# Performance work log

Hardware: AMD Instinct MI355X
Metric: run time of the kernel (lower is better)

Reference implementation:

```python
import jax, jax.numpy as jnp
import numpy as np
from jax import lax

# physiological constants from the source module
DT = 1.0
TAU_L = 10.0
G_B = 0.6
G_L = 1.0 / TAU_L
LAMBDA_MAX = 0.35
STEPS = int(50 / DT)

IN_SIZE, HID, OUT, BATCH = 1024, 2048, 512, 4096


def setup_inputs() -> dict:
    key = jax.random.key(0)
    k1, k2, k3, k4, k5, k6 = jax.random.split(key, 6)
    psp = jax.random.uniform(k1, (IN_SIZE, BATCH), dtype=jnp.float32)  # |mm(spikes,kernel)| is >=0
    label = jax.random.uniform(k2, (BATCH, OUT), dtype=jnp.float32)    # teaching current I
    # Linear params init: uniform(-0.1, 0.1) as in the torch module
    W_h = jax.random.uniform(k3, (HID, IN_SIZE), minval=-0.1, maxval=0.1, dtype=jnp.float32)
    b_h = jax.random.uniform(k4, (HID,), minval=-0.1, maxval=0.1, dtype=jnp.float32)
    W_o = jax.random.uniform(k5, (OUT, HID), minval=-0.1, maxval=0.1, dtype=jnp.float32)
    b_o = jax.random.uniform(k6, (OUT,), minval=-0.1, maxval=0.1, dtype=jnp.float32)
    return {"psp": psp, "label": label, "W_h": W_h, "b_h": b_h, "W_o": W_o, "b_o": b_o}


def reference(psp, label, W_h, b_h, W_o, b_o):
    a = DT / TAU_L
    gr = G_B / G_L  # = 6.0
    x = psp.T  # [B, in] -- Hidden_layer transposes basal_input
    # psp is constant over the time loop, so the hidden basal GEMM hoists out
    basal_V_h = x @ W_h.T + b_h  # [B, HID]
    soma_h0 = jnp.zeros_like(basal_V_h)
    soma_o0 = jnp.zeros((x.shape[0], W_o.shape[0]), dtype=x.dtype)

    def step(carry, _):
        soma_h, soma_o = carry
        # hidden two-compartment leaky integration
        soma_h = soma_h + a * (-soma_h + gr * (basal_V_h - soma_h))
        rate_h = LAMBDA_MAX * jax.nn.sigmoid(soma_h)  # [B, HID]
        basal_V_o = rate_h @ W_o.T + b_o              # [B, OUT]
        # output layer, training (test=False) branch: nudged by teaching current I=label
        soma_o = soma_o + a * (-soma_o + gr * (basal_V_o - soma_o) + label - soma_o)
        return (soma_h, soma_o), None

    (soma_h, soma_o), _ = lax.scan(step, (soma_h0, soma_o0), None, length=STEPS)
    return LAMBDA_MAX * jax.nn.sigmoid(soma_o)  # out_layer.spike_rate, [B, OUT]
```

## Files before the change

### kernel.cpp

```cpp
#include <hip/hip_runtime.h>
#include <hip/hip_bf16.h>


typedef __bf16 bf16_t;
typedef __bf16 bf16x8 __attribute__((ext_vector_type(8)));
typedef __bf16 bf16x4v __attribute__((ext_vector_type(4)));
typedef float f32x4 __attribute__((ext_vector_type(4)));
typedef float f32x16 __attribute__((ext_vector_type(16)));

#define GLD_TO_LDS16(gp, lp)                                            \
  __builtin_amdgcn_global_load_lds(                                     \
      (__attribute__((address_space(1))) void*)(void*)(gp),             \
      (__attribute__((address_space(3))) void*)(lp), 16, 0, 0)

__global__ __launch_bounds__(256) void prep(
    const float* __restrict__ psp, bf16_t* __restrict__ pspT,
    const float4* __restrict__ w1, bf16x4v* __restrict__ o1, int n1,
    const float4* __restrict__ w2, bf16x4v* __restrict__ o2, int n2) {
  __shared__ float tile[64][65];
  const int tid = threadIdx.x;
  const int b = blockIdx.x;
  const int c0 = (b & 63) * 64;
  const int r0 = (b >> 6) * 64;
  const int tx = tid & 63;
  const int ty = tid >> 6;
#pragma unroll
  for (int i = 0; i < 16; ++i) {
    const int r = ty + i * 4;
    tile[r][tx] = psp[(size_t)(r0 + r) * 4096 + c0 + tx];
  }
  const int base = b * 768 + tid;
#pragma unroll
  for (int i = 0; i < 3; ++i) {
    const int idx = base + i * 256;
    const float4 v = (idx < n1) ? w1[idx] : w2[idx - n1];
    bf16x4v o;
    o.x = (bf16_t)v.x; o.y = (bf16_t)v.y; o.z = (bf16_t)v.z; o.w = (bf16_t)v.w;
    if (idx < n1) o1[idx] = o;
    else if (idx - n1 < n2) o2[idx - n1] = o;
  }
  __syncthreads();
#pragma unroll
  for (int i = 0; i < 16; ++i) {
    const int r = ty + i * 4;
    pspT[(size_t)(c0 + r) * 1024 + r0 + tx] = (bf16_t)tile[tx][r];
  }
}

__global__ __launch_bounds__(256, 4) void gemm1_nt(
    const bf16_t* __restrict__ A, const bf16_t* __restrict__ Bt,
    const float* __restrict__ bias, bf16_t* __restrict__ C,
    int M, int N, int K) {
  constexpr int BK = 64;
  __shared__ __align__(16) bf16_t sA[128 * BK];
  __shared__ __align__(16) bf16_t sB[64 * BK];

  const int tid = threadIdx.x;
  const int wave = tid >> 6;
  const int lane = tid & 63;
  const int bm = blockIdx.x * 128;
  const int bn = blockIdx.y * 64;
  const int wm = (wave & 1) * 64;
  const int wn = (wave >> 1) * 32;

  f32x16 acc[2] = {};

  const int srow8 = lane >> 3;
  const int gseg = (lane & 7) ^ srow8;
  const bf16_t* Ag = A + (size_t)(bm + wave * 32 + srow8) * K + gseg * 8;
  const bf16_t* Bg = Bt + (size_t)(bn + wave * 16 + srow8) * K + gseg * 8;
  const int dstA = wave * 2048;
  const int dstB = wave * 1024;

  const int col = lane & 31;
  const int g = lane >> 5;

  for (int k0 = 0; k0 < K; k0 += BK) {
#pragma unroll
    for (int c = 0; c < 4; ++c)
      GLD_TO_LDS16(Ag + (size_t)(c * 8) * K + k0, sA + dstA + c * 512);
#pragma unroll
    for (int c = 0; c < 2; ++c)
      GLD_TO_LDS16(Bg + (size_t)(c * 8) * K + k0, sB + dstB + c * 512);
    __syncthreads();

#pragma unroll
    for (int ks = 0; ks < 4; ++ks) {
      const int q = ks * 2 + g;
      bf16x8 av[2], bv;
#pragma unroll
      for (int i = 0; i < 2; ++i) {
        const int rr = wm + i * 32 + col;
        av[i] = *(const bf16x8*)(sA + rr * BK + ((q ^ (rr & 7)) * 8));
      }
      {
        const int rr = wn + col;
        bv = *(const bf16x8*)(sB + rr * BK + ((q ^ (rr & 7)) * 8));
      }
#pragma unroll
      for (int i = 0; i < 2; ++i)
        acc[i] = __builtin_amdgcn_mfma_f32_32x32x16_bf16(av[i], bv, acc[i],
                                                         0, 0, 0);
    }
    __syncthreads();
  }

  const int rbase = 4 * g;
  const int gn = bn + wn + col;
  const float bj = bias[gn];
#pragma unroll
  for (int i = 0; i < 2; ++i) {
#pragma unroll
    for (int r = 0; r < 16; ++r) {
      const int gm = bm + wm + i * 32 + (r & 3) + 8 * (r >> 2) + rbase;
      const float z = 0.8571428571428571f * (acc[i][r] + bj);
      C[(size_t)gm * N + gn] = (bf16_t)(0.35f / (1.0f + __expf(-z)));
    }
  }
}

__global__ __launch_bounds__(256, 4) void gemm2_nt(
    const bf16_t* __restrict__ A, const bf16_t* __restrict__ Bt,
    const float* __restrict__ bias, const float* __restrict__ lbl,
    float* __restrict__ out, int M, int N, int K) {
  __shared__ __align__(16) bf16_t sA[2][64 * 64];
  __shared__ __align__(16) bf16_t sB[2][64 * 64];

  const int tid = threadIdx.x;
  const int wave = tid >> 6;
  const int lane = tid & 63;
  const int bm = blockIdx.x * 64;
  const int bn = blockIdx.y * 64;
  const int wm = (wave & 1) * 32;
  const int wn = (wave >> 1) * 32;

  f32x4 acc[2][2] = {};

  const int srow8 = lane >> 3;
  const int gseg = (lane & 7) ^ srow8;
  const bf16_t* Ag = A + (size_t)(bm + wave * 16 + srow8) * K + gseg * 8;
  const bf16_t* Bg = Bt + (size_t)(bn + wave * 16 + srow8) * K + gseg * 8;
  const int dst = wave * 1024;

  const int fr = lane & 15;
  const int qh = lane >> 4;

  for (int k0 = 0; k0 < K; k0 += 128) {
#pragma unroll
    for (int p = 0; p < 2; ++p) {
#pragma unroll
      for (int c = 0; c < 2; ++c) {
        GLD_TO_LDS16(Ag + k0 + p * 64 + (size_t)(c * 8) * K,
                     sA[p] + dst + c * 512);
        GLD_TO_LDS16(Bg + k0 + p * 64 + (size_t)(c * 8) * K,
                     sB[p] + dst + c * 512);
      }
    }
    __syncthreads();

#pragma unroll
    for (int ks = 0; ks < 4; ++ks) {
      const int q = ks * 4 + qh;
      const int pnl = q >> 3;
      const int q2 = q & 7;
      bf16x8 av[2], bv[2];
#pragma unroll
      for (int i = 0; i < 2; ++i) {
        const int ra = wm + i * 16 + fr;
        av[i] = *(const bf16x8*)(sA[pnl] + ra * 64 + ((q2 ^ (ra & 7)) * 8));
      }
#pragma unroll
      for (int j = 0; j < 2; ++j) {
        const int rb = wn + j * 16 + fr;
        bv[j] = *(const bf16x8*)(sB[pnl] + rb * 64 + ((q2 ^ (rb & 7)) * 8));
      }
#pragma unroll
      for (int i = 0; i < 2; ++i)
#pragma unroll
        for (int j = 0; j < 2; ++j)
          acc[i][j] = __builtin_amdgcn_mfma_f32_16x16x32_bf16(
              av[i], bv[j], acc[i][j], 0, 0, 0);
    }
    __syncthreads();
  }

  const int cm0 = qh * 4;
#pragma unroll
  for (int j = 0; j < 2; ++j) {
    const int gn = bn + wn + j * 16 + fr;
    const float bj = bias[gn];
#pragma unroll
    for (int i = 0; i < 2; ++i) {
#pragma unroll
      for (int r = 0; r < 4; ++r) {
        const int gm = bm + wm + i * 16 + cm0 + r;
        const float z =
            0.75f * (acc[i][j][r] + bj) + 0.125f * lbl[(size_t)gm * N + gn];
        out[(size_t)gm * N + gn] = 0.35f / (1.0f + __expf(-z));
      }
    }
  }
}

extern "C" void kernel_launch(void* const* d_in, const int* in_sizes, int n_in,
                              void* d_out, int out_size, void* d_ws, size_t ws_size,
                              hipStream_t stream) {
  constexpr int IN = 1024, HID = 2048, OUT = 512, B = 4096;
  const float* psp = (const float*)d_in[0];
  const float* lbl = (const float*)d_in[1];
  const float* W_h = (const float*)d_in[2];
  const float* b_h = (const float*)d_in[3];
  const float* W_o = (const float*)d_in[4];
  const float* b_o = (const float*)d_in[5];
  float* out = (float*)d_out;

  bf16_t* Whb = (bf16_t*)d_ws;
  bf16_t* Wob = Whb + (size_t)HID * IN;
  bf16_t* pspT = Wob + (size_t)OUT * HID;
  bf16_t* Rm = pspT + (size_t)B * IN;

  prep<<<1024, 256, 0, stream>>>(
      psp, pspT, (const float4*)W_h, (bf16x4v*)Whb, HID * IN / 4,
      (const float4*)W_o, (bf16x4v*)Wob, OUT * HID / 4);
  gemm1_nt<<<dim3(B / 128, HID / 64), 256, 0, stream>>>(
      pspT, Whb, b_h, Rm, B, HID, IN);
  gemm2_nt<<<dim3(B / 64, OUT / 64), 256, 0, stream>>>(
      Rm, Wob, b_o, lbl, out, B, OUT, HID);
}
```

Measured before the change: 129.3 us.

## Enlarge gemm1 tile to 128x256 with triple-buffered LDS pipeline

gemm1 now uses 512-thread blocks, each computing a 128x256 output tile instead of 128x64, with eight waves each owning a 64x64 sub-tile. Global-to-LDS loads for tile t+2 are issued in three chunks interleaved with the four MFMA phases of tile t, using a three-stage LDS ring buffer, explicit vmcnt waits, barriers and setprio around the MFMAs. The intent is to hide global-load latency and raise arithmetic intensity. The cost is more LDS per block, lower occupancy, and hand-tuned waitcnt ordering that could be fragile.

```diff
diff --git a/kernel.cpp b/kernel.cpp
--- a/kernel.cpp
+++ b/kernel.cpp
@@ -47,74 +47,141 @@
   }
 }
 
-__global__ __launch_bounds__(256, 4) void gemm1_nt(
+__global__ __launch_bounds__(512, 2) void gemm1_nt(
     const bf16_t* __restrict__ A, const bf16_t* __restrict__ Bt,
     const float* __restrict__ bias, bf16_t* __restrict__ C,
     int M, int N, int K) {
   constexpr int BK = 64;
-  __shared__ __align__(16) bf16_t sA[128 * BK];
-  __shared__ __align__(16) bf16_t sB[64 * BK];
+  __shared__ __align__(16) bf16_t sA[3][128 * BK];
+  __shared__ __align__(16) bf16_t sB[3][256 * BK];
 
   const int tid = threadIdx.x;
   const int wave = tid >> 6;
   const int lane = tid & 63;
   const int bm = blockIdx.x * 128;
-  const int bn = blockIdx.y * 64;
+  const int bn = blockIdx.y * 256;
   const int wm = (wave & 1) * 64;
-  const int wn = (wave >> 1) * 32;
-
-  f32x16 acc[2] = {};
+  const int wn = (wave >> 1) * 64;
+
+  f32x16 acc[2][2] = {};
 
   const int srow8 = lane >> 3;
   const int gseg = (lane & 7) ^ srow8;
-  const bf16_t* Ag = A + (size_t)(bm + wave * 32 + srow8) * K + gseg * 8;
-  const bf16_t* Bg = Bt + (size_t)(bn + wave * 16 + srow8) * K + gseg * 8;
-  const int dstA = wave * 2048;
-  const int dstB = wave * 1024;
+  const bf16_t* Ag = A + (size_t)(bm + wave * 16 + srow8) * K + gseg * 8;
+  const bf16_t* Bg = Bt + (size_t)(bn + wave * 32 + srow8) * K + gseg * 8;
+  const int dstA = wave * 1024;
+  const int dstB = wave * 2048;
 
   const int col = lane & 31;
   const int g = lane >> 5;
-
-  for (int k0 = 0; k0 < K; k0 += BK) {
-#pragma unroll
-    for (int c = 0; c < 4; ++c)
-      GLD_TO_LDS16(Ag + (size_t)(c * 8) * K + k0, sA + dstA + c * 512);
-#pragma unroll
-    for (int c = 0; c < 2; ++c)
-      GLD_TO_LDS16(Bg + (size_t)(c * 8) * K + k0, sB + dstB + c * 512);
-    __syncthreads();
-
-#pragma unroll
-    for (int ks = 0; ks < 4; ++ks) {
-      const int q = ks * 2 + g;
-      bf16x8 av[2], bv;
-#pragma unroll
-      for (int i = 0; i < 2; ++i) {
-        const int rr = wm + i * 32 + col;
-        av[i] = *(const bf16x8*)(sA + rr * BK + ((q ^ (rr & 7)) * 8));
-      }
-      {
-        const int rr = wn + col;
-        bv = *(const bf16x8*)(sB + rr * BK + ((q ^ (rr & 7)) * 8));
-      }
-#pragma unroll
-      for (int i = 0; i < 2; ++i)
-        acc[i] = __builtin_amdgcn_mfma_f32_32x32x16_bf16(av[i], bv, acc[i],
-                                                         0, 0, 0);
-    }
-    __syncthreads();
-  }
+  const int NT = K / BK;
+
+#define STAGE_A2(bufi, t)                                              \
+  {                                                                    \
+    bf16_t* d_ = &sA[bufi][dstA];                                      \
+    const bf16_t* s_ = Ag + (size_t)(t) * BK;                          \
+    GLD_TO_LDS16(s_, d_);                                              \
+    GLD_TO_LDS16(s_ + (size_t)8 * K, d_ + 512);                        \
+  }
+#define STAGE_B01(bufi, t)                                             \
+  {                                                                    \
+    bf16_t* d_ = &sB[bufi][dstB];                                      \
+    const bf16_t* s_ = Bg + (size_t)(t) * BK;                          \
+    GLD_TO_LDS16(s_, d_);                                              \
+    GLD_TO_LDS16(s_ + (size_t)8 * K, d_ + 512);                        \
+  }
+#define STAGE_B23(bufi, t)                                             \
+  {                                                                    \
+    bf16_t* d_ = &sB[bufi][dstB + 1024];                               \
+    const bf16_t* s_ = Bg + (size_t)(t) * BK + (size_t)16 * K;         \
+    GLD_TO_LDS16(s_, d_);                                              \
+    GLD_TO_LDS16(s_ + (size_t)8 * K, d_ + 512);                        \
+  }
+#define PH_READ(ks)                                                    \
+  {                                                                    \
+    const int q = (ks) * 2 + g;                                        \
+    _Pragma("unroll") for (int i = 0; i < 2; ++i) {                    \
+      const int rr = wm + i * 32 + col;                                \
+      av[i] = *(const bf16x8*)(a_ + rr * BK + ((q ^ (rr & 7)) * 8));   \
+    }                                                                  \
+    _Pragma("unroll") for (int j = 0; j < 2; ++j) {                    \
+      const int rr = wn + j * 32 + col;                                \
+      bv[j] = *(const bf16x8*)(b_ + rr * BK + ((q ^ (rr & 7)) * 8));   \
+    }                                                                  \
+  }
+#define PH_MFMA()                                                      \
+  __builtin_amdgcn_s_setprio(1);                                       \
+  _Pragma("unroll") for (int i = 0; i < 2; ++i)                        \
+      _Pragma("unroll") for (int j = 0; j < 2; ++j)                    \
+          acc[i][j] = __builtin_amdgcn_mfma_f32_32x32x16_bf16(         \
+              av[i], bv[j], acc[i][j], 0, 0, 0);                       \
+  __builtin_amdgcn_s_setprio(0);
+#define SYNC_PRE()                                                     \
+  __builtin_amdgcn_sched_barrier(0);                                   \
+  __builtin_amdgcn_s_barrier();                                        \
+  asm volatile("s_waitcnt lgkmcnt(0)" ::: "memory");                   \
+  __builtin_amdgcn_sched_barrier(0);
+#define SYNC_POST()                                                    \
+  __builtin_amdgcn_sched_barrier(0);                                   \
+  __builtin_amdgcn_s_barrier();                                        \
+  __builtin_amdgcn_sched_barrier(0);
+
+  STAGE_A2(0, 0); STAGE_B01(0, 0); STAGE_B23(0, 0);
+  STAGE_A2(1, 1); STAGE_B01(1, 1); STAGE_B23(1, 1);
+  asm volatile("s_waitcnt vmcnt(6)" ::: "memory");
+  __builtin_amdgcn_sched_barrier(0);
+  __builtin_amdgcn_s_barrier();
+  __builtin_amdgcn_sched_barrier(0);
+
+  int cur = 0;
+  for (int t = 0; t < NT; ++t) {
+    const bf16_t* a_ = sA[cur];
+    const bf16_t* b_ = sB[cur];
+    const int nxt = (cur >= 1) ? cur - 1 : cur + 2;
+    const bool st = (t + 2) < NT;
+    bf16x8 av[2], bv[2];
+
+    PH_READ(0);
+    if (st) STAGE_A2(nxt, t + 2);
+    SYNC_PRE(); PH_MFMA(); SYNC_POST();
+    PH_READ(1);
+    if (st) STAGE_B01(nxt, t + 2);
+    SYNC_PRE(); PH_MFMA(); SYNC_POST();
+    PH_READ(2);
+    if (st) STAGE_B23(nxt, t + 2);
+    SYNC_PRE(); PH_MFMA(); SYNC_POST();
+    PH_READ(3);
+    if (t + 1 < NT) {
+      if (t + 2 < NT)
+        asm volatile("s_waitcnt vmcnt(6)" ::: "memory");
+      else
+        asm volatile("s_waitcnt vmcnt(0)" ::: "memory");
+    }
+    SYNC_PRE(); PH_MFMA(); SYNC_POST();
+
+    cur = (cur + 1 == 3) ? 0 : cur + 1;
+  }
+#undef STAGE_A2
+#undef STAGE_B01
+#undef STAGE_B23
+#undef PH_READ
+#undef PH_MFMA
+#undef SYNC_PRE
+#undef SYNC_POST
 
   const int rbase = 4 * g;
-  const int gn = bn + wn + col;
-  const float bj = bias[gn];
-#pragma unroll
-  for (int i = 0; i < 2; ++i) {
-#pragma unroll
-    for (int r = 0; r < 16; ++r) {
-      const int gm = bm + wm + i * 32 + (r & 3) + 8 * (r >> 2) + rbase;
-      const float z = 0.8571428571428571f * (acc[i][r] + bj);
-      C[(size_t)gm * N + gn] = (bf16_t)(0.35f / (1.0f + __expf(-z)));
+#pragma unroll
+  for (int j = 0; j < 2; ++j) {
+    const int gn = bn + wn + j * 32 + col;
+    const float bj = bias[gn];
+#pragma unroll
+    for (int i = 0; i < 2; ++i) {
+#pragma unroll
+      for (int r = 0; r < 16; ++r) {
+        const int gm = bm + wm + i * 32 + (r & 3) + 8 * (r >> 2) + rbase;
+        const float z = 0.8571428571428571f * (acc[i][j][r] + bj);
+        C[(size_t)gm * N + gn] = (bf16_t)(0.35f / (1.0f + __expf(-z)));
+      }
     }
   }
 }
@@ -222,7 +289,7 @@
   prep<<<1024, 256, 0, stream>>>(
       psp, pspT, (const float4*)W_h, (bf16x4v*)Whb, HID * IN / 4,
       (const float4*)W_o, (bf16x4v*)Wob, OUT * HID / 4);
-  gemm1_nt<<<dim3(B / 128, HID / 64), 256, 0, stream>>>(
+  gemm1_nt<<<dim3(B / 128, HID / 256), 512, 0, stream>>>(
       pspT, Whb, b_h, Rm, B, HID, IN);
   gemm2_nt<<<dim3(B / 64, OUT / 64), 256, 0, stream>>>(
       Rm, Wob, b_o, lbl, out, B, OUT, HID);
```

Result: slower. 132.1 us (+2.1%).

## Double-buffer LDS tiles in both GEMMs to overlap global loads with MFMA

Applied to the files above, without the earlier changes.

Both GEMM kernels now use two LDS buffers. The next K-tile is issued with global_load_lds before the current tile's MFMAs run, and each iteration ends with a single waitcnt plus barrier instead of two syncthreads. MFMA sections are wrapped in s_setprio, and launch-bound occupancy hints are lowered to match the larger LDS footprint. The aim is to hide global load latency behind compute, at the cost of more LDS per block and fewer resident blocks per CU.

```diff
diff --git a/kernel.cpp b/kernel.cpp
--- a/kernel.cpp
+++ b/kernel.cpp
@@ -12,6 +12,12 @@
   __builtin_amdgcn_global_load_lds(                                     \
       (__attribute__((address_space(1))) void*)(void*)(gp),             \
       (__attribute__((address_space(3))) void*)(lp), 16, 0, 0)
+
+#define END_OF_ITER_SYNC()                                              \
+  asm volatile("s_waitcnt vmcnt(0)" ::: "memory");                      \
+  __builtin_amdgcn_sched_barrier(0);                                    \
+  __builtin_amdgcn_s_barrier();                                         \
+  __builtin_amdgcn_sched_barrier(0);
 
 __global__ __launch_bounds__(256) void prep(
     const float* __restrict__ psp, bf16_t* __restrict__ pspT,
@@ -47,13 +53,13 @@
   }
 }
 
-__global__ __launch_bounds__(256, 4) void gemm1_nt(
+__global__ __launch_bounds__(256, 3) void gemm1_nt(
     const bf16_t* __restrict__ A, const bf16_t* __restrict__ Bt,
     const float* __restrict__ bias, bf16_t* __restrict__ C,
     int M, int N, int K) {
   constexpr int BK = 64;
-  __shared__ __align__(16) bf16_t sA[128 * BK];
-  __shared__ __align__(16) bf16_t sB[64 * BK];
+  __shared__ __align__(16) bf16_t sA[2][128 * BK];
+  __shared__ __align__(16) bf16_t sB[2][64 * BK];
 
   const int tid = threadIdx.x;
   const int wave = tid >> 6;
@@ -74,16 +80,29 @@
 
   const int col = lane & 31;
   const int g = lane >> 5;
-
-  for (int k0 = 0; k0 < K; k0 += BK) {
-#pragma unroll
-    for (int c = 0; c < 4; ++c)
-      GLD_TO_LDS16(Ag + (size_t)(c * 8) * K + k0, sA + dstA + c * 512);
-#pragma unroll
-    for (int c = 0; c < 2; ++c)
-      GLD_TO_LDS16(Bg + (size_t)(c * 8) * K + k0, sB + dstB + c * 512);
-    __syncthreads();
-
+  const int NT = K / BK;
+
+#define STAGE1(bufi, t)                                                \
+  {                                                                    \
+    bf16_t* dA_ = &sA[bufi][dstA];                                     \
+    bf16_t* dB_ = &sB[bufi][dstB];                                     \
+    const bf16_t* sa_ = Ag + (size_t)(t) * BK;                         \
+    const bf16_t* sb_ = Bg + (size_t)(t) * BK;                         \
+    _Pragma("unroll") for (int c_ = 0; c_ < 4; ++c_)                   \
+        GLD_TO_LDS16(sa_ + (size_t)(c_ * 8) * K, dA_ + c_ * 512);      \
+    _Pragma("unroll") for (int c_ = 0; c_ < 2; ++c_)                   \
+        GLD_TO_LDS16(sb_ + (size_t)(c_ * 8) * K, dB_ + c_ * 512);      \
+  }
+
+  STAGE1(0, 0);
+  END_OF_ITER_SYNC();
+
+  int cur = 0;
+  for (int t = 0; t < NT; ++t) {
+    if (t + 1 < NT) STAGE1(cur ^ 1, t + 1);
+
+    const bf16_t* a_ = sA[cur];
+    const bf16_t* b_ = sB[cur];
 #pragma unroll
     for (int ks = 0; ks < 4; ++ks) {
       const int q = ks * 2 + g;
@@ -91,19 +110,26 @@
 #pragma unroll
       for (int i = 0; i < 2; ++i) {
         const int rr = wm + i * 32 + col;
-        av[i] = *(const bf16x8*)(sA + rr * BK + ((q ^ (rr & 7)) * 8));
+        av[i] = *(const bf16x8*)(a_ + rr * BK + ((q ^ (rr & 7)) * 8));
       }
       {
         const int rr = wn + col;
-        bv = *(const bf16x8*)(sB + rr * BK + ((q ^ (rr & 7)) * 8));
-      }
+        bv = *(const bf16x8*)(b_ + rr * BK + ((q ^ (rr & 7)) * 8));
+      }
+      __builtin_amdgcn_s_setprio(1);
 #pragma unroll
       for (int i = 0; i < 2; ++i)
         acc[i] = __builtin_amdgcn_mfma_f32_32x32x16_bf16(av[i], bv, acc[i],
                                                          0, 0, 0);
-    }
-    __syncthreads();
-  }
+      __builtin_amdgcn_s_setprio(0);
+    }
+
+    if (t + 1 < NT) {
+      END_OF_ITER_SYNC();
+      cur ^= 1;
+    }
+  }
+#undef STAGE1
 
   const int rbase = 4 * g;
   const int gn = bn + wn + col;
@@ -119,12 +145,12 @@
   }
 }
 
-__global__ __launch_bounds__(256, 4) void gemm2_nt(
+__global__ __launch_bounds__(256, 2) void gemm2_nt(
     const bf16_t* __restrict__ A, const bf16_t* __restrict__ Bt,
     const float* __restrict__ bias, const float* __restrict__ lbl,
     float* __restrict__ out, int M, int N, int K) {
-  __shared__ __align__(16) bf16_t sA[2][64 * 64];
-  __shared__ __align__(16) bf16_t sB[2][64 * 64];
+  __shared__ __align__(16) bf16_t sA[2][2][64 * 64];
+  __shared__ __align__(16) bf16_t sB[2][2][64 * 64];
 
   const int tid = threadIdx.x;
   const int wave = tid >> 6;
@@ -144,45 +170,66 @@
 
   const int fr = lane & 15;
   const int qh = lane >> 4;
-
-  for (int k0 = 0; k0 < K; k0 += 128) {
-#pragma unroll
-    for (int p = 0; p < 2; ++p) {
-#pragma unroll
-      for (int c = 0; c < 2; ++c) {
-        GLD_TO_LDS16(Ag + k0 + p * 64 + (size_t)(c * 8) * K,
-                     sA[p] + dst + c * 512);
-        GLD_TO_LDS16(Bg + k0 + p * 64 + (size_t)(c * 8) * K,
-                     sB[p] + dst + c * 512);
-      }
-    }
-    __syncthreads();
-
+  const int NT = K / 128;
+
+#define STAGE2(bufi, t)                                                \
+  {                                                                    \
+    const int k0_ = (t) * 128;                                         \
+    _Pragma("unroll") for (int p_ = 0; p_ < 2; ++p_) {                 \
+      _Pragma("unroll") for (int c_ = 0; c_ < 2; ++c_) {               \
+        GLD_TO_LDS16(Ag + k0_ + p_ * 64 + (size_t)(c_ * 8) * K,        \
+                     sA[bufi][p_] + dst + c_ * 512);                   \
+        GLD_TO_LDS16(Bg + k0_ + p_ * 64 + (size_t)(c_ * 8) * K,        \
+                     sB[bufi][p_] + dst + c_ * 512);                   \
+      }                                                                \
+    }                                                                  \
+  }
+
+  STAGE2(0, 0);
+  END_OF_ITER_SYNC();
+
+  int cur = 0;
+  for (int t = 0; t < NT; ++t) {
+    if (t + 1 < NT) STAGE2(cur ^ 1, t + 1);
+
+    const bf16_t* a0 = sA[cur][0];
+    const bf16_t* a1 = sA[cur][1];
+    const bf16_t* b0 = sB[cur][0];
+    const bf16_t* b1 = sB[cur][1];
 #pragma unroll
     for (int ks = 0; ks < 4; ++ks) {
       const int q = ks * 4 + qh;
-      const int pnl = q >> 3;
+      const int pnl = ks >> 1;
       const int q2 = q & 7;
+      const bf16_t* aP = pnl ? a1 : a0;
+      const bf16_t* bP = pnl ? b1 : b0;
       bf16x8 av[2], bv[2];
 #pragma unroll
       for (int i = 0; i < 2; ++i) {
         const int ra = wm + i * 16 + fr;
-        av[i] = *(const bf16x8*)(sA[pnl] + ra * 64 + ((q2 ^ (ra & 7)) * 8));
+        av[i] = *(const bf16x8*)(aP + ra * 64 + ((q2 ^ (ra & 7)) * 8));
       }
 #pragma unroll
       for (int j = 0; j < 2; ++j) {
         const int rb = wn + j * 16 + fr;
-        bv[j] = *(const bf16x8*)(sB[pnl] + rb * 64 + ((q2 ^ (rb & 7)) * 8));
-      }
+        bv[j] = *(const bf16x8*)(bP + rb * 64 + ((q2 ^ (rb & 7)) * 8));
+      }
+      __builtin_amdgcn_s_setprio(1);
 #pragma unroll
       for (int i = 0; i < 2; ++i)
 #pragma unroll
         for (int j = 0; j < 2; ++j)
           acc[i][j] = __builtin_amdgcn_mfma_f32_16x16x32_bf16(
               av[i], bv[j], acc[i][j], 0, 0, 0);
-    }
-    __syncthreads();
-  }
+      __builtin_amdgcn_s_setprio(0);
+    }
+
+    if (t + 1 < NT) {
+      END_OF_ITER_SYNC();
+      cur ^= 1;
+    }
+  }
+#undef STAGE2
 
   const int cm0 = qh * 4;
 #pragma unroll
```

New measurement: 137.2 us. 1.06x slower.
